# Optimization experiments

Measured on AMD Instinct MI355X. Metric: run time of the kernel, lower is better.

The kernel has to match this reference:

```python
import jax, jax.numpy as jnp
import numpy as np

SEQ_LEN, BATCH, INPUT, HIDDEN, N_OUT = 512, 128, 512, 1024, 4


def setup_inputs() -> dict:
    key = jax.random.key(0)
    ks = jax.random.split(key, 8)
    s_ih = 1.0 / np.sqrt(HIDDEN)
    inp = {
        "inputs": jax.random.normal(ks[0], (SEQ_LEN, BATCH, INPUT), dtype=jnp.float32),
        "h0": jnp.zeros((BATCH, HIDDEN), dtype=jnp.float32),
        "c0": jnp.zeros((BATCH, HIDDEN), dtype=jnp.float32),
        # PyTorch LSTMCell params: weight_ih [4H, I], weight_hh [4H, H], biases [4H]
        "W_ih": jax.random.uniform(ks[1], (4 * HIDDEN, INPUT), jnp.float32, -s_ih, s_ih),
        "W_hh": jax.random.uniform(ks[2], (4 * HIDDEN, HIDDEN), jnp.float32, -s_ih, s_ih),
        "b_ih": jax.random.uniform(ks[3], (4 * HIDDEN,), jnp.float32, -s_ih, s_ih),
        "b_hh": jax.random.uniform(ks[4], (4 * HIDDEN,), jnp.float32, -s_ih, s_ih),
        "W_dec": jax.random.uniform(ks[5], (N_OUT, HIDDEN), jnp.float32, -s_ih, s_ih),
        "b_dec": jax.random.uniform(ks[6], (N_OUT,), jnp.float32, -s_ih, s_ih),
    }
    return inp


def reference(inputs, h0, c0, W_ih, W_hh, b_ih, b_hh, W_dec, b_dec):
    # Precompute input projections for all timesteps in one big GEMM:
    # [S, B, I] @ [I, 4H] -> [S, B, 4H]
    x_proj = jnp.einsum('sbi,gi->sbg', inputs, W_ih) + b_ih + b_hh

    def step(carry, xp):
        h, c = carry
        gates = xp + h @ W_hh.T  # [B, 4H]
        i, f, g, o = jnp.split(gates, 4, axis=-1)  # PyTorch gate order i,f,g,o
        i = jax.nn.sigmoid(i)
        f = jax.nn.sigmoid(f)
        g = jnp.tanh(g)
        o = jax.nn.sigmoid(o)
        c_new = f * c + i * g
        h_new = o * jnp.tanh(c_new)
        return (h_new, c_new), None

    (h_last, _), _ = jax.lax.scan(step, (h0, c0), x_proj)
    logits = h_last @ W_dec.T + b_dec  # [B, 4]
    # Original applies nn.Softmax(dim=0), i.e. over the batch dimension.
    return jax.nn.softmax(logits, axis=0)
```

## Files before the change

kernel.cpp:

```cpp
#include <hip/hip_runtime.h>
#include <math.h>

#define SEQ   512
#define BATCH 128
#define INP   512
#define HID   1024
#define G4    4096
#define NOUT  4
#define GO_IDX 384

typedef short bf16x8 __attribute__((ext_vector_type(8)));
typedef float f32x4  __attribute__((ext_vector_type(4)));

__device__ __forceinline__ unsigned short f2bf(float x) {
  unsigned int u = __float_as_uint(x);
  unsigned int r = (u + 0x7FFFu + ((u >> 16) & 1u)) >> 16;
  return (unsigned short)r;
}
__device__ __forceinline__ float bf2f(unsigned short h) {
  return __uint_as_float(((unsigned int)h) << 16);
}

__device__ __forceinline__ bf16x8 ld_h16_uc(const unsigned short* p) {
  union { unsigned long long q[2]; bf16x8 v; } u;
  unsigned long long* pp = (unsigned long long*)(void*)p;
  u.q[0] = __hip_atomic_load(pp,     __ATOMIC_RELAXED, __HIP_MEMORY_SCOPE_SYSTEM);
  u.q[1] = __hip_atomic_load(pp + 1, __ATOMIC_RELAXED, __HIP_MEMORY_SCOPE_SYSTEM);
  return u.v;
}

__global__ void prepack_w(const float* __restrict__ W,
                          unsigned short* __restrict__ Whi,
                          unsigned short* __restrict__ Wlo) {
  int T = blockIdx.x * blockDim.x + threadIdx.x;
  int L = T & 63;
  int kstep = (T >> 6) & 31;
  int bk = T >> 11;
  int m = L & 15, q = L >> 4;
  int row = (m & 3) * HID + bk * 4 + (m >> 2);
  int k = kstep * 32 + q * 8;
  const float* src = W + (size_t)row * HID + k;
  unsigned short hi[8], lo[8];
#pragma unroll
  for (int i = 0; i < 8; i++) {
    float x = src[i];
    unsigned short h = f2bf(x);
    hi[i] = h;
    lo[i] = f2bf(x - bf2f(h));
  }
  size_t o = (size_t)T * 8;
#pragma unroll
  for (int i = 0; i < 8; i++) { Whi[o + i] = hi[i]; Wlo[o + i] = lo[i]; }
}

__global__ void init_state(const float* __restrict__ h0, const float* __restrict__ c0,
                           unsigned short* __restrict__ hhi, unsigned short* __restrict__ hlo,
                           float* __restrict__ cT, unsigned int* __restrict__ flags) {
  int idx = blockIdx.x * blockDim.x + threadIdx.x;
  if (idx < 512) flags[idx] = 0u;
  int b = idx >> 10;
  int j = idx & (HID - 1);
  float x = h0[idx];
  unsigned short h = f2bf(x);
  hhi[idx] = h;
  hlo[idx] = f2bf(x - bf2f(h));
  cT[j * BATCH + b] = c0[idx];
}

__global__ void transpose_in(const float* __restrict__ in, float* __restrict__ xt,
                             int nrows) {
  __shared__ float s[32][33];
  int tx = threadIdx.x & 31, ty = threadIdx.x >> 5;
  int n0 = blockIdx.x * 32, i0 = blockIdx.y * 32;
#pragma unroll
  for (int r = 0; r < 4; r++) {
    int n = n0 + ty + 8 * r;
    s[ty + 8 * r][tx] = in[(size_t)n * INP + i0 + tx];
  }
  __syncthreads();
#pragma unroll
  for (int r = 0; r < 4; r++) {
    int i = i0 + ty + 8 * r;
    xt[(size_t)i * nrows + n0 + tx] = s[tx][ty + 8 * r];
  }
}

__global__ __launch_bounds__(256, 3)
void gemm_xproj(const float* __restrict__ A, const float* __restrict__ Bm,
                const float* __restrict__ b_ih, const float* __restrict__ b_hh,
                float* __restrict__ C, int N) {
  __shared__ float As[32][128];
  __shared__ float Bs[32][128];
  int t = threadIdx.x;
  int g0 = blockIdx.x * 128;
  int n0 = blockIdx.y * 128;
  int mg = (t >> 4) * 8, nn = (t & 15) * 8;
  float acc[8][8] = {};
  for (int k0 = 0; k0 < INP; k0 += 32) {
#pragma unroll
    for (int r = 0; r < 4; r++) {
      int idx = t + 256 * r;
      int g = idx >> 3, i4 = idx & 7;
      float4 v = *(const float4*)&A[(size_t)(g0 + g) * INP + k0 + 4 * i4];
      As[4 * i4 + 0][g] = v.x; As[4 * i4 + 1][g] = v.y;
      As[4 * i4 + 2][g] = v.z; As[4 * i4 + 3][g] = v.w;
    }
#pragma unroll
    for (int r = 0; r < 4; r++) {
      int idx = t + 256 * r;
      int kk = idx >> 5, n4 = idx & 31;
      *(float4*)&Bs[kk][4 * n4] = *(const float4*)&Bm[(size_t)(k0 + kk) * N + n0 + 4 * n4];
    }
    __syncthreads();
#pragma unroll 4
    for (int kk = 0; kk < 32; kk++) {
      float4 a0 = *(const float4*)&As[kk][mg];
      float4 a1 = *(const float4*)&As[kk][mg + 4];
      float4 bb0 = *(const float4*)&Bs[kk][nn];
      float4 bb1 = *(const float4*)&Bs[kk][nn + 4];
      float av[8] = {a0.x, a0.y, a0.z, a0.w, a1.x, a1.y, a1.z, a1.w};
      float bv[8] = {bb0.x, bb0.y, bb0.z, bb0.w, bb1.x, bb1.y, bb1.z, bb1.w};
#pragma unroll
      for (int i2 = 0; i2 < 8; i2++)
#pragma unroll
        for (int j2 = 0; j2 < 8; j2++)
          acc[i2][j2] = fmaf(av[i2], bv[j2], acc[i2][j2]);
    }
    __syncthreads();
  }
#pragma unroll
  for (int i2 = 0; i2 < 8; i2++) {
    int g = g0 + mg + i2;
    float bias = b_ih[g] + b_hh[g];
#pragma unroll
    for (int j2 = 0; j2 < 8; j2++) {
      C[(size_t)g * N + n0 + nn + j2] = acc[i2][j2] + bias;
    }
  }
}

__global__ __launch_bounds__(256)
void lstm_seq(const unsigned short* __restrict__ Whi,
              const unsigned short* __restrict__ Wlo,
              const float* __restrict__ XP, int N, int CT, int step0,
              unsigned short* __restrict__ h0hi, unsigned short* __restrict__ h0lo,
              unsigned short* __restrict__ h1hi, unsigned short* __restrict__ h1lo,
              float* __restrict__ cT, unsigned int* flags) {
  __shared__ bf16x8 Wlds[8192];
  __shared__ unsigned short hstage[64][2][8];

  int bk = blockIdx.x;
  int jblk = bk >> 1;
  int bh2 = bk & 1;
  int t = threadIdx.x;
  int w = t >> 6;
  int L = t & 63;
  int n = L & 15, q = L >> 4;
  int b = bh2 * 64 + w * 16 + n;
  int j0 = jblk * 8 + q;

  {
    float4* ldsf = (float4*)Wlds;
    const float4* s1 = (const float4*)(Whi + (size_t)jblk * 32768);
    const float4* s2 = (const float4*)(Wlo + (size_t)jblk * 32768);
#pragma unroll
    for (int i = 0; i < 16; i++) ldsf[t + 256 * i] = s1[t + 256 * i];
#pragma unroll
    for (int i = 0; i < 16; i++) ldsf[4096 + t + 256 * i] = s2[t + 256 * i];
  }

  int ci0 = j0 * BATCH + b;
  int ci1 = (j0 + 4) * BATCH + b;
  float cc0 = cT[ci0];
  float cc1 = cT[ci1];

  size_t hoff = (size_t)b * HID + q * 8;

  int r_bl   = t >> 2;
  int r_arr  = (t >> 1) & 1;
  int r_half = t & 1;
  size_t r_off = (size_t)(bh2 * 64 + r_bl) * HID + jblk * 8 + r_half * 4;

  __syncthreads();

  for (int tt = 0; tt < CT; tt++) {
    int gs = step0 + tt;
    int odd = gs & 1;
    const unsigned short* Bh = (odd ? h1hi : h0hi) + hoff;
    const unsigned short* Bl = (odd ? h1lo : h0lo) + hoff;
    unsigned short* dhi = odd ? h0hi : h1hi;
    unsigned short* dlo = odd ? h0lo : h1lo;
    const float* xpc = XP + (size_t)tt * BATCH;

    float xpv0[4], xpv1[4];
#pragma unroll
    for (int g = 0; g < 4; g++) {
      xpv0[g] = xpc[(size_t)(g * HID + j0) * N + b];
      xpv1[g] = xpc[(size_t)(g * HID + j0 + 4) * N + b];
    }

    f32x4 acc0 = {0.f, 0.f, 0.f, 0.f};
    f32x4 acc1 = {0.f, 0.f, 0.f, 0.f};
#pragma unroll 8
    for (int ks = 0; ks < 32; ks++) {
      bf16x8 bhv = ld_h16_uc(Bh + ks * 32);
      bf16x8 blv = ld_h16_uc(Bl + ks * 32);
      bf16x8 ah0 = Wlds[ks * 64 + L];
      bf16x8 ah1 = Wlds[2048 + ks * 64 + L];
      bf16x8 al0 = Wlds[4096 + ks * 64 + L];
      bf16x8 al1 = Wlds[6144 + ks * 64 + L];
      acc0 = __builtin_amdgcn_mfma_f32_16x16x32_bf16(ah0, bhv, acc0, 0, 0, 0);
      acc1 = __builtin_amdgcn_mfma_f32_16x16x32_bf16(ah1, bhv, acc1, 0, 0, 0);
      acc0 = __builtin_amdgcn_mfma_f32_16x16x32_bf16(ah0, blv, acc0, 0, 0, 0);
      acc1 = __builtin_amdgcn_mfma_f32_16x16x32_bf16(ah1, blv, acc1, 0, 0, 0);
      acc0 = __builtin_amdgcn_mfma_f32_16x16x32_bf16(al0, bhv, acc0, 0, 0, 0);
      acc1 = __builtin_amdgcn_mfma_f32_16x16x32_bf16(al1, bhv, acc1, 0, 0, 0);
    }

    {
      float i_ = 1.f / (1.f + expf(-(acc0[0] + xpv0[0])));
      float f_ = 1.f / (1.f + expf(-(acc0[1] + xpv0[1])));
      float g_ = tanhf(acc0[2] + xpv0[2]);
      float o_ = 1.f / (1.f + expf(-(acc0[3] + xpv0[3])));
      cc0 = f_ * cc0 + i_ * g_;
      float hn = o_ * tanhf(cc0);
      unsigned short hh = f2bf(hn);
      hstage[w * 16 + n][0][q] = hh;
      hstage[w * 16 + n][1][q] = f2bf(hn - bf2f(hh));
    }
    {
      float i_ = 1.f / (1.f + expf(-(acc1[0] + xpv1[0])));
      float f_ = 1.f / (1.f + expf(-(acc1[1] + xpv1[1])));
      float g_ = tanhf(acc1[2] + xpv1[2]);
      float o_ = 1.f / (1.f + expf(-(acc1[3] + xpv1[3])));
      cc1 = f_ * cc1 + i_ * g_;
      float hn = o_ * tanhf(cc1);
      unsigned short hh = f2bf(hn);
      hstage[w * 16 + n][0][q + 4] = hh;
      hstage[w * 16 + n][1][q + 4] = f2bf(hn - bf2f(hh));
    }

    __syncthreads();

    {
      unsigned long long v =
          *(const unsigned long long*)&hstage[r_bl][r_arr][r_half * 4];
      unsigned short* basep = r_arr ? dlo : dhi;
      __hip_atomic_store((unsigned long long*)(void*)(basep + r_off), v,
                         __ATOMIC_RELAXED, __HIP_MEMORY_SCOPE_SYSTEM);
    }

    unsigned tgt = (unsigned)(gs + 1);
    __syncthreads();
    if (t == 0)
      __hip_atomic_store(&flags[bk], tgt, __ATOMIC_RELAXED,
                         __HIP_MEMORY_SCOPE_SYSTEM);
    if (bk == 0) {
      unsigned gcnt = 0;
      while (__hip_atomic_load(&flags[t], __ATOMIC_RELAXED,
                               __HIP_MEMORY_SCOPE_SYSTEM) < tgt &&
             ++gcnt < (1u << 16))
        __builtin_amdgcn_s_sleep(1);
      __syncthreads();
      if (t == 0)
        __hip_atomic_store(&flags[GO_IDX], tgt, __ATOMIC_RELAXED,
                           __HIP_MEMORY_SCOPE_SYSTEM);
    } else if (t == 0) {
      unsigned gcnt = 0;
      while (__hip_atomic_load(&flags[GO_IDX], __ATOMIC_RELAXED,
                               __HIP_MEMORY_SCOPE_SYSTEM) < tgt &&
             ++gcnt < (1u << 16))
        __builtin_amdgcn_s_sleep(1);
    }
    __syncthreads();
  }

  cT[ci0] = cc0;
  cT[ci1] = cc1;
}

__global__ void decode_softmax(const unsigned short* __restrict__ hhi,
                               const unsigned short* __restrict__ hlo,
                               const float* __restrict__ Wd,
                               const float* __restrict__ bd, float* __restrict__ out) {
  __shared__ float lg[NOUT][BATCH];
  __shared__ float mx[NOUT], sm[NOUT];
  int t = threadIdx.x;
  int b = t >> 2, o = t & 3;
  float s = bd[o];
  for (int j = 0; j < HID; j++) {
    float hv = bf2f(hhi[(size_t)b * HID + j]) + bf2f(hlo[(size_t)b * HID + j]);
    s += hv * Wd[o * HID + j];
  }
  lg[o][b] = s;
  __syncthreads();
  if (t < NOUT) {
    float m = -1e30f;
    for (int b2 = 0; b2 < BATCH; b2++) m = fmaxf(m, lg[t][b2]);
    float ss = 0.f;
    for (int b2 = 0; b2 < BATCH; b2++) ss += expf(lg[t][b2] - m);
    mx[t] = m; sm[t] = ss;
  }
  __syncthreads();
  out[b * NOUT + o] = expf(lg[o][b] - mx[o]) / sm[o];
}

extern "C" void kernel_launch(void* const* d_in, const int* in_sizes, int n_in,
                              void* d_out, int out_size, void* d_ws, size_t ws_size,
                              hipStream_t stream) {
  const float* inputs = (const float*)d_in[0];
  const float* h0     = (const float*)d_in[1];
  const float* c0     = (const float*)d_in[2];
  const float* W_ih   = (const float*)d_in[3];
  const float* W_hh   = (const float*)d_in[4];
  const float* b_ih   = (const float*)d_in[5];
  const float* b_hh   = (const float*)d_in[6];
  const float* W_dec  = (const float*)d_in[7];
  const float* b_dec  = (const float*)d_in[8];
  float* out = (float*)d_out;

  char* w = (char*)d_ws;
  unsigned short* Whi = (unsigned short*)w;  w += (size_t)G4 * HID * 2;
  unsigned short* Wlo = (unsigned short*)w;  w += (size_t)G4 * HID * 2;
  unsigned short* hhi[2], *hlo[2];
  hhi[0] = (unsigned short*)w;  w += (size_t)BATCH * HID * 2;
  hhi[1] = (unsigned short*)w;  w += (size_t)BATCH * HID * 2;
  hlo[0] = (unsigned short*)w;  w += (size_t)BATCH * HID * 2;
  hlo[1] = (unsigned short*)w;  w += (size_t)BATCH * HID * 2;
  float* cT = (float*)w;        w += (size_t)HID * BATCH * 4;
  unsigned int* flags = (unsigned int*)w;  w += 2048;
  size_t used = (size_t)(w - (char*)d_ws);

  size_t per_ct = ((size_t)INP * BATCH + (size_t)G4 * BATCH) * 4;
  int CT = 1;
  if (ws_size > used) {
    size_t avail = (ws_size - used) / per_ct;
    for (int c = SEQ; c >= 1; c >>= 1)
      if ((size_t)c <= avail) { CT = c; break; }
  }
  float* Xt = (float*)w;  w += (size_t)INP * BATCH * CT * 4;
  float* XP = (float*)w;
  int N = CT * BATCH;

  prepack_w<<<(256 * 32 * 64) / 256, 256, 0, stream>>>(W_hh, Whi, Wlo);
  init_state<<<BATCH * HID / 256, 256, 0, stream>>>(h0, c0, hhi[0], hlo[0], cT, flags);

  for (int t0 = 0; t0 < SEQ; t0 += CT) {
    transpose_in<<<dim3(N / 32, INP / 32), 256, 0, stream>>>(
        inputs + (size_t)t0 * BATCH * INP, Xt, N);
    gemm_xproj<<<dim3(G4 / 128, N / 128), 256, 0, stream>>>(
        W_ih, Xt, b_ih, b_hh, XP, N);

    int Nv = N, CTv = CT, step0 = t0;
    void* kargs[] = {
        (void*)&Whi, (void*)&Wlo, (void*)&XP, (void*)&Nv, (void*)&CTv,
        (void*)&step0, (void*)&hhi[0], (void*)&hlo[0], (void*)&hhi[1],
        (void*)&hlo[1], (void*)&cT, (void*)&flags};
    hipLaunchCooperativeKernel((const void*)lstm_seq, dim3(256), dim3(256),
                               kargs, 0, stream);
  }

  decode_softmax<<<1, 512, 0, stream>>>(hhi[0], hlo[0], W_dec, b_dec, out);
}
```

Before: 12.50 ms.

## Prefetch next-step input projections and spread grid-barrier release flags

Moves the per-timestep load of precomputed input projections ahead of the step: the next step's values are loaded before the grid barrier wait, so global-load latency overlaps the spin. The single global 'go' flag is replaced by eight copies on separate cache lines, each polled by a subset of blocks, to reduce contention when many blocks spin on one address. The staging buffer is padded to change LDS bank mapping, and prepack writes are fused into one loop. The flag region doubles in size.

Measured after the change: 12.50 ms. No clear change (-0.0%).

```diff
diff --git a/kernel.cpp b/kernel.cpp
--- a/kernel.cpp
+++ b/kernel.cpp
@@ -7,7 +7,6 @@
 #define HID   1024
 #define G4    4096
 #define NOUT  4
-#define GO_IDX 384
 
 typedef short bf16x8 __attribute__((ext_vector_type(8)));
 typedef float f32x4  __attribute__((ext_vector_type(4)));
@@ -40,24 +39,21 @@
   int row = (m & 3) * HID + bk * 4 + (m >> 2);
   int k = kstep * 32 + q * 8;
   const float* src = W + (size_t)row * HID + k;
-  unsigned short hi[8], lo[8];
+  size_t o = (size_t)T * 8;
 #pragma unroll
   for (int i = 0; i < 8; i++) {
     float x = src[i];
     unsigned short h = f2bf(x);
-    hi[i] = h;
-    lo[i] = f2bf(x - bf2f(h));
-  }
-  size_t o = (size_t)T * 8;
-#pragma unroll
-  for (int i = 0; i < 8; i++) { Whi[o + i] = hi[i]; Wlo[o + i] = lo[i]; }
+    Whi[o + i] = h;
+    Wlo[o + i] = f2bf(x - bf2f(h));
+  }
 }
 
 __global__ void init_state(const float* __restrict__ h0, const float* __restrict__ c0,
                            unsigned short* __restrict__ hhi, unsigned short* __restrict__ hlo,
                            float* __restrict__ cT, unsigned int* __restrict__ flags) {
   int idx = blockIdx.x * blockDim.x + threadIdx.x;
-  if (idx < 512) flags[idx] = 0u;
+  if (idx < 1024) flags[idx] = 0u;
   int b = idx >> 10;
   int j = idx & (HID - 1);
   float x = h0[idx];
@@ -147,7 +143,7 @@
               unsigned short* __restrict__ h1hi, unsigned short* __restrict__ h1lo,
               float* __restrict__ cT, unsigned int* flags) {
   __shared__ bf16x8 Wlds[8192];
-  __shared__ unsigned short hstage[64][2][8];
+  __shared__ unsigned short hstage[64][2][12];
 
   int bk = blockIdx.x;
   int jblk = bk >> 1;
@@ -183,6 +179,13 @@
 
   __syncthreads();
 
+  float xa0[4], xa1[4];
+#pragma unroll
+  for (int g = 0; g < 4; g++) {
+    xa0[g] = XP[(size_t)(g * HID + j0) * N + b];
+    xa1[g] = XP[(size_t)(g * HID + j0 + 4) * N + b];
+  }
+
   for (int tt = 0; tt < CT; tt++) {
     int gs = step0 + tt;
     int odd = gs & 1;
@@ -190,14 +193,6 @@
     const unsigned short* Bl = (odd ? h1lo : h0lo) + hoff;
     unsigned short* dhi = odd ? h0hi : h1hi;
     unsigned short* dlo = odd ? h0lo : h1lo;
-    const float* xpc = XP + (size_t)tt * BATCH;
-
-    float xpv0[4], xpv1[4];
-#pragma unroll
-    for (int g = 0; g < 4; g++) {
-      xpv0[g] = xpc[(size_t)(g * HID + j0) * N + b];
-      xpv1[g] = xpc[(size_t)(g * HID + j0 + 4) * N + b];
-    }
 
     f32x4 acc0 = {0.f, 0.f, 0.f, 0.f};
     f32x4 acc1 = {0.f, 0.f, 0.f, 0.f};
@@ -218,10 +213,10 @@
     }
 
     {
-      float i_ = 1.f / (1.f + expf(-(acc0[0] + xpv0[0])));
-      float f_ = 1.f / (1.f + expf(-(acc0[1] + xpv0[1])));
-      float g_ = tanhf(acc0[2] + xpv0[2]);
-      float o_ = 1.f / (1.f + expf(-(acc0[3] + xpv0[3])));
+      float i_ = 1.f / (1.f + expf(-(acc0[0] + xa0[0])));
+      float f_ = 1.f / (1.f + expf(-(acc0[1] + xa0[1])));
+      float g_ = tanhf(acc0[2] + xa0[2]);
+      float o_ = 1.f / (1.f + expf(-(acc0[3] + xa0[3])));
       cc0 = f_ * cc0 + i_ * g_;
       float hn = o_ * tanhf(cc0);
       unsigned short hh = f2bf(hn);
@@ -229,10 +224,10 @@
       hstage[w * 16 + n][1][q] = f2bf(hn - bf2f(hh));
     }
     {
-      float i_ = 1.f / (1.f + expf(-(acc1[0] + xpv1[0])));
-      float f_ = 1.f / (1.f + expf(-(acc1[1] + xpv1[1])));
-      float g_ = tanhf(acc1[2] + xpv1[2]);
-      float o_ = 1.f / (1.f + expf(-(acc1[3] + xpv1[3])));
+      float i_ = 1.f / (1.f + expf(-(acc1[0] + xa1[0])));
+      float f_ = 1.f / (1.f + expf(-(acc1[1] + xa1[1])));
+      float g_ = tanhf(acc1[2] + xa1[2]);
+      float o_ = 1.f / (1.f + expf(-(acc1[3] + xa1[3])));
       cc1 = f_ * cc1 + i_ * g_;
       float hn = o_ * tanhf(cc1);
       unsigned short hh = f2bf(hn);
@@ -248,6 +243,17 @@
       unsigned short* basep = r_arr ? dlo : dhi;
       __hip_atomic_store((unsigned long long*)(void*)(basep + r_off), v,
                          __ATOMIC_RELAXED, __HIP_MEMORY_SCOPE_SYSTEM);
+    }
+
+    float xb0[4], xb1[4];
+    {
+      int tpf = (tt + 1 < CT) ? (tt + 1) : tt;
+      const float* xpc = XP + (size_t)tpf * BATCH;
+#pragma unroll
+      for (int g = 0; g < 4; g++) {
+        xb0[g] = xpc[(size_t)(g * HID + j0) * N + b];
+        xb1[g] = xpc[(size_t)(g * HID + j0 + 4) * N + b];
+      }
     }
 
     unsigned tgt = (unsigned)(gs + 1);
@@ -262,17 +268,21 @@
              ++gcnt < (1u << 16))
         __builtin_amdgcn_s_sleep(1);
       __syncthreads();
-      if (t == 0)
-        __hip_atomic_store(&flags[GO_IDX], tgt, __ATOMIC_RELAXED,
+      if (t < 8)
+        __hip_atomic_store(&flags[512 + t * 32], tgt, __ATOMIC_RELAXED,
                            __HIP_MEMORY_SCOPE_SYSTEM);
     } else if (t == 0) {
       unsigned gcnt = 0;
-      while (__hip_atomic_load(&flags[GO_IDX], __ATOMIC_RELAXED,
+      const unsigned int* gop = &flags[512 + (bk & 7) * 32];
+      while (__hip_atomic_load(gop, __ATOMIC_RELAXED,
                                __HIP_MEMORY_SCOPE_SYSTEM) < tgt &&
              ++gcnt < (1u << 16))
         __builtin_amdgcn_s_sleep(1);
     }
     __syncthreads();
+
+#pragma unroll
+    for (int g = 0; g < 4; g++) { xa0[g] = xb0[g]; xa1[g] = xb1[g]; }
   }
 
   cT[ci0] = cc0;
@@ -328,7 +338,7 @@
   hlo[0] = (unsigned short*)w;  w += (size_t)BATCH * HID * 2;
   hlo[1] = (unsigned short*)w;  w += (size_t)BATCH * HID * 2;
   float* cT = (float*)w;        w += (size_t)HID * BATCH * 4;
-  unsigned int* flags = (unsigned int*)w;  w += 2048;
+  unsigned int* flags = (unsigned int*)w;  w += 4096;
   size_t used = (size_t)(w - (char*)d_ws);
 
   size_t per_ct = ((size_t)INP * BATCH + (size_t)G4 * BATCH) * 4;
```
